# Optimization experiments

Measured on AMD Instinct MI355X. Metric: run time of the kernel, lower is better.

Reference implementation:

```python
import jax, jax.numpy as jnp
import numpy as np


def setup_inputs() -> dict:
    key = jax.random.key(0)
    ks = jax.random.split(key, 5)
    B, Lq, Lkv, HQ, H, D, S, BS = 1, 256, 4096, 32, 2, 128, 16, 64
    q = jax.random.normal(ks[0], (B, Lq, HQ, D), jnp.float32)
    k = jax.random.normal(ks[1], (B, Lkv, H, D), jnp.float32)
    v = jax.random.normal(ks[2], (B, Lkv, H, D), jnp.float32)
    w = jax.random.uniform(ks[3], (B, Lq, HQ, S), jnp.float32)
    block_indices = jax.random.randint(ks[4], (B, Lq, H, S), 0, Lkv // BS).astype(jnp.int32)
    return {"q": q, "k": k, "v": v, "w": w, "block_indices": block_indices, "block_size": BS}


def reference(q, k, v, w, block_indices, block_size):
    # q: (B, Lq, HQ, D); k,v: (B, Lkv, H, D); w: (B, Lq, HQ, num_weights);
    # block_indices: (B, Lq, H, S) int32, entries < 0 are skipped.
    B, Lq, HQ, D = q.shape
    H = k.shape[2]
    S = block_indices.shape[-1]
    G = HQ // H  # query heads per kv head
    nb = k.shape[1] // block_size
    sm_scale = 1.0 / (D ** 0.5)  # default scale in the kernel

    # Reshape KV into blocks: (B, H, nb, BS, D)
    kb = k.reshape(B, nb, block_size, H, D).transpose(0, 3, 1, 2, 4)
    vb = v.reshape(B, nb, block_size, H, D).transpose(0, 3, 1, 2, 4)

    idx = block_indices.transpose(0, 2, 1, 3)  # (B, H, Lq, S)
    valid = idx >= 0
    idx = jnp.maximum(idx, 0)

    # Gather selected blocks per (batch, kv_head): -> (B, H, Lq, S, BS, D)
    gather = jax.vmap(jax.vmap(lambda blocks, ind: blocks[ind]))
    kg = gather(kb, idx)
    vg = gather(vb, idx)

    # Group query heads by kv head: (B, H, Lq, G, D)
    qh = q.reshape(B, Lq, H, G, D).transpose(0, 2, 1, 3, 4)

    # Per-block scores and per-block softmax over the BS keys (axis u)
    scores = jnp.einsum('bhlgd,bhlsud->bhlgsu', qh, kg) * sm_scale
    p = jax.nn.softmax(scores, axis=-1)

    # Per-(head, block) learned weight; only first S weights of w are used.
    wh = w[..., :S].reshape(B, Lq, H, G, S).transpose(0, 2, 1, 3, 4)  # (B,H,Lq,G,S)
    coef = wh * valid[:, :, :, None, :].astype(p.dtype)
    p = p * coef[..., None]

    o = jnp.einsum('bhlgsu,bhlsud->bhlgd', p, vg)  # (B, H, Lq, G, D)
    return o.transpose(0, 2, 1, 3, 4).reshape(B, Lq, HQ, D)
```

## Files before the change

### kernel.cpp

```cpp
#include <hip/hip_runtime.h>
#include <hip/hip_bf16.h>


namespace {

constexpr int kLq = 256, kHQ = 32, kH = 2, kG = 16, kD = 128, kS = 16;
constexpr int kNB = 64;
constexpr float kScaleLog2e = 0.08838834764831845f * 1.4426950408889634f;

constexpr int kKPackN = kH * kNB * 16 * 64;
constexpr int kPStr   = 72;
constexpr int kSStr   = 136;

typedef short s16x8 __attribute__((ext_vector_type(8)));
typedef float f32x4 __attribute__((ext_vector_type(4)));

union U32BF2 { unsigned int u; __hip_bfloat162 h; };
union FragU  { uint4 u; s16x8 v; };

static __device__ inline unsigned int pk_bf16(float a, float b) {
    U32BF2 z; z.h = __float22bfloat162_rn(make_float2(a, b));
    return z.u;
}

__global__ __launch_bounds__(256)
void pack_kv(const float* __restrict__ k, const float* __restrict__ v,
             uint4* __restrict__ kp, uint4* __restrict__ vp)
{
    __shared__ unsigned short S_s[64 * kSStr];

    const int bid  = blockIdx.x;
    const int isV  = bid & 1;
    const int blk  = (bid >> 1) & 63;
    const int h    = bid >> 7;
    const int t    = threadIdx.x;
    const int lane = t & 63, n = lane & 15, quad = lane >> 4;
    const int wv   = t >> 6;

    {
        const float* src = (isV ? v : k) + ((size_t)blk * 64 * kH + h) * kD;
        const int r0 = t >> 5, c4 = (t & 31) << 2;
        #pragma unroll
        for (int p = 0; p < 8; ++p) {
            const int r = p * 8 + r0;
            const float4 f = *(const float4*)(src + (size_t)r * (kH * kD) + c4);
            *(unsigned int*)&S_s[r * kSStr + c4]     = pk_bf16(f.x, f.y);
            *(unsigned int*)&S_s[r * kSStr + c4 + 2] = pk_bf16(f.z, f.w);
        }
    }
    __syncthreads();

    const size_t obase = (size_t)(h * 64 + blk) * 16 * 64;
    if (!isV) {
        #pragma unroll
        for (int rep = 0; rep < 4; ++rep) {
            const int u = wv * 16 + n;
            kp[obase + (size_t)(wv * 4 + rep) * 64 + lane] =
                *(const uint4*)&S_s[u * kSStr + rep * 32 + quad * 8];
        }
    } else {
        #pragma unroll
        for (int rep = 0; rep < 4; ++rep) {
            const int c  = wv * 4 + rep;
            const int d  = (c >> 1) * 16 + n;
            const int u0 = (c & 1) * 32 + quad * 8;
            unsigned short s[8];
            #pragma unroll
            for (int j = 0; j < 8; ++j) s[j] = S_s[(u0 + j) * kSStr + d];
            uint4 val;
            val.x = s[0] | ((unsigned)s[1] << 16);
            val.y = s[2] | ((unsigned)s[3] << 16);
            val.z = s[4] | ((unsigned)s[5] << 16);
            val.w = s[6] | ((unsigned)s[7] << 16);
            vp[obase + (size_t)c * 64 + lane] = val;
        }
    }
}

__global__ __launch_bounds__(256, 2)
void hsa_main(const float* __restrict__ q, const float* __restrict__ w,
              const int* __restrict__ bidx, const uint4* __restrict__ kp,
              const uint4* __restrict__ vp, float* __restrict__ out)
{
    __shared__ __align__(16) unsigned short P_s[4 * kG * kPStr];
    __shared__ float O_red[kD * 17];

    const int bid  = blockIdx.x;
    const int l    = bid >> 1;
    const int h    = bid & 1;
    const int tid  = threadIdx.x;
    const int wave = tid >> 6;
    const int lane = tid & 63;
    const int n    = lane & 15;
    const int quad = lane >> 4;

    for (int i = tid; i < kD * 17; i += 256) O_red[i] = 0.f;

    s16x8 qf[4];
    {
        const float* qb = q + ((size_t)l * kHQ + h * kG + n) * kD + quad * 8;
        #pragma unroll
        for (int st = 0; st < 4; ++st) {
            const float4 f0 = *(const float4*)(qb + st * 32);
            const float4 f1 = *(const float4*)(qb + st * 32 + 4);
            union { s16x8 v; unsigned int u[4]; } z;
            z.u[0] = pk_bf16(f0.x, f0.y); z.u[1] = pk_bf16(f0.z, f0.w);
            z.u[2] = pk_bf16(f1.x, f1.y); z.u[3] = pk_bf16(f1.z, f1.w);
            qf[st] = z.v;
        }
    }

    const int4   bis = *(const int4*)(bidx + (size_t)(l * kH + h) * kS + wave * 4);
    const float4 wv4 = *(const float4*)(w + ((size_t)l * kHQ + h * kG + n) * kS + wave * 4);
    int   base_[4];
    float wval[4];
    {
        const int b[4] = {bis.x, bis.y, bis.z, bis.w};
        const float ww[4] = {wv4.x, wv4.y, wv4.z, wv4.w};
        #pragma unroll
        for (int j = 0; j < 4; ++j) {
            wval[j]  = (b[j] < 0) ? 0.f : ww[j];
            base_[j] = (h * kNB + max(b[j], 0)) * 16 * 64;
        }
    }

    __syncthreads();

    unsigned short* Pw = &P_s[wave * kG * kPStr];
    f32x4 oacc[8];
    #pragma unroll
    for (int dt = 0; dt < 8; ++dt) oacc[dt] = (f32x4){0.f, 0.f, 0.f, 0.f};

    FragU kreg[16];
    #pragma unroll
    for (int i = 0; i < 16; ++i) kreg[i].u = kp[base_[0] + i * 64 + lane];
    __builtin_amdgcn_sched_barrier(0);

    #pragma unroll
    for (int js = 0; js < 4; ++js) {
        FragU vreg[16];
        #pragma unroll
        for (int i = 0; i < 16; ++i) vreg[i].u = vp[base_[js] + i * 64 + lane];
        __builtin_amdgcn_sched_barrier(0);

        f32x4 sc[4];
        #pragma unroll
        for (int t = 0; t < 4; ++t) sc[t] = (f32x4){0.f, 0.f, 0.f, 0.f};
        #pragma unroll
        for (int t = 0; t < 4; ++t)
            #pragma unroll
            for (int st = 0; st < 4; ++st)
                sc[t] = __builtin_amdgcn_mfma_f32_16x16x32_bf16(
                    kreg[t * 4 + st].v, qf[st], sc[t], 0, 0, 0);

        if (js < 3) {
            #pragma unroll
            for (int i = 0; i < 16; ++i) kreg[i].u = kp[base_[js + 1] + i * 64 + lane];
        }
        __builtin_amdgcn_sched_barrier(0);

        float part = 0.f;
        #pragma unroll
        for (int t = 0; t < 4; ++t)
            #pragma unroll
            for (int r = 0; r < 4; ++r) {
                sc[t][r] = exp2f(sc[t][r] * kScaleLog2e);
                part += sc[t][r];
            }
        part += __shfl_xor(part, 16);
        part += __shfl_xor(part, 32);
        const float coef = wval[js] / part;

        #pragma unroll
        for (int t = 0; t < 4; ++t) {
            const unsigned long long pq =
                ((unsigned long long)pk_bf16(sc[t][2] * coef, sc[t][3] * coef) << 32) |
                pk_bf16(sc[t][0] * coef, sc[t][1] * coef);
            *(unsigned long long*)&Pw[n * kPStr + t * 16 + quad * 4] = pq;
        }
        const s16x8 bf0 = *(const s16x8*)&Pw[n * kPStr + quad * 8];
        const s16x8 bf1 = *(const s16x8*)&Pw[n * kPStr + 32 + quad * 8];

        #pragma unroll
        for (int dt = 0; dt < 8; ++dt) {
            oacc[dt] = __builtin_amdgcn_mfma_f32_16x16x32_bf16(
                vreg[dt * 2 + 0].v, bf0, oacc[dt], 0, 0, 0);
            oacc[dt] = __builtin_amdgcn_mfma_f32_16x16x32_bf16(
                vreg[dt * 2 + 1].v, bf1, oacc[dt], 0, 0, 0);
        }
        __builtin_amdgcn_sched_barrier(0);
    }

    #pragma unroll
    for (int dt = 0; dt < 8; ++dt)
        #pragma unroll
        for (int r = 0; r < 4; ++r)
            atomicAdd(&O_red[(dt * 16 + quad * 4 + r) * 17 + n], oacc[dt][r]);

    __syncthreads();

    {
        float* ob = out + ((size_t)l * kHQ + h * kG) * kD;
        #pragma unroll
        for (int rep = 0; rep < 2; ++rep) {
            const int idx = rep * 256 + tid;
            const int g = idx >> 5, d0 = (idx & 31) << 2;
            const float4 val = make_float4(O_red[(d0 + 0) * 17 + g],
                                           O_red[(d0 + 1) * 17 + g],
                                           O_red[(d0 + 2) * 17 + g],
                                           O_red[(d0 + 3) * 17 + g]);
            *(float4*)(ob + (size_t)g * kD + d0) = val;
        }
    }
}

}

extern "C" void kernel_launch(void* const* d_in, const int* in_sizes, int n_in,
                              void* d_out, int out_size, void* d_ws, size_t ws_size,
                              hipStream_t stream)
{
    const float* q    = (const float*)d_in[0];
    const float* k    = (const float*)d_in[1];
    const float* v    = (const float*)d_in[2];
    const float* w    = (const float*)d_in[3];
    const int*   bidx = (const int*)d_in[4];
    float* out = (float*)d_out;

    uint4* kp = (uint4*)d_ws;
    uint4* vp = (uint4*)((char*)d_ws + (size_t)kKPackN * 16);

    pack_kv<<<dim3(256), dim3(256), 0, stream>>>(k, v, kp, vp);
    hsa_main<<<dim3(kLq * kH), dim3(256), 0, stream>>>(q, w, bidx, kp, vp, out);
}
```

Before: 105.7 us.

## Double-buffer K/V blocks in LDS via async loads and split D across waves

Instead of each wave owning 4 of the 16 selected blocks and loading K/V fragments into registers, all four waves cooperatively stream each block into a double-buffered LDS staging area using global_load_lds. The next block is fetched while the current one is computed. Each wave then computes the full QK scores redundantly and owns a 32-wide slice of the output D dimension, which removes the LDS atomic cross-wave reduction and the O_red buffer. The trade-off is redundant score MFMAs and softmax in every wave, plus a block-wide barrier per selected block. The barrier between issuing the async loads and consuming the buffer relies on __syncthreads to also wait on the outstanding loads.

```diff
diff --git a/kernel.cpp b/kernel.cpp
--- a/kernel.cpp
+++ b/kernel.cpp
@@ -16,7 +16,6 @@
 typedef float f32x4 __attribute__((ext_vector_type(4)));
 
 union U32BF2 { unsigned int u; __hip_bfloat162 h; };
-union FragU  { uint4 u; s16x8 v; };
 
 static __device__ inline unsigned int pk_bf16(float a, float b) {
     U32BF2 z; z.h = __float22bfloat162_rn(make_float2(a, b));
@@ -82,8 +81,8 @@
               const int* __restrict__ bidx, const uint4* __restrict__ kp,
               const uint4* __restrict__ vp, float* __restrict__ out)
 {
+    __shared__ __align__(16) uint4 buf[2][32 * 64];
     __shared__ __align__(16) unsigned short P_s[4 * kG * kPStr];
-    __shared__ float O_red[kD * 17];
 
     const int bid  = blockIdx.x;
     const int l    = bid >> 1;
@@ -94,8 +93,6 @@
     const int n    = lane & 15;
     const int quad = lane >> 4;
 
-    for (int i = tid; i < kD * 17; i += 256) O_red[i] = 0.f;
-
     s16x8 qf[4];
     {
         const float* qb = q + ((size_t)l * kHQ + h * kG + n) * kD + quad * 8;
@@ -110,38 +107,52 @@
         }
     }
 
-    const int4   bis = *(const int4*)(bidx + (size_t)(l * kH + h) * kS + wave * 4);
-    const float4 wv4 = *(const float4*)(w + ((size_t)l * kHQ + h * kG + n) * kS + wave * 4);
-    int   base_[4];
-    float wval[4];
-    {
-        const int b[4] = {bis.x, bis.y, bis.z, bis.w};
-        const float ww[4] = {wv4.x, wv4.y, wv4.z, wv4.w};
-        #pragma unroll
-        for (int j = 0; j < 4; ++j) {
-            wval[j]  = (b[j] < 0) ? 0.f : ww[j];
-            base_[j] = (h * kNB + max(b[j], 0)) * 16 * 64;
-        }
-    }
-
+    int   base_[kS];
+    float wval[kS];
+    #pragma unroll
+    for (int i = 0; i < 4; ++i) {
+        const int4   b4 = *(const int4*)(bidx + (size_t)(l * kH + h) * kS + i * 4);
+        const float4 w4 = *(const float4*)(w + ((size_t)l * kHQ + h * kG + n) * kS + i * 4);
+        const int   bb[4] = {b4.x, b4.y, b4.z, b4.w};
+        const float ww[4] = {w4.x, w4.y, w4.z, w4.w};
+        #pragma unroll
+        for (int jj = 0; jj < 4; ++jj) {
+            wval[i * 4 + jj]  = (bb[jj] < 0) ? 0.f : ww[jj];
+            base_[i * 4 + jj] = (h * kNB + max(bb[jj], 0)) * 1024;
+        }
+    }
+
+    const int    f0    = wave * 8;
+    const uint4* gsrc  = (f0 < 16) ? kp : vp;
+    const int    fbase = (f0 < 16) ? f0 * 64 : (f0 - 16) * 64;
+
+    #define STAGE(js_, b_)                                                     \
+        {                                                                      \
+            const uint4* gp = gsrc + base_[(js_)] + fbase + lane;              \
+            auto* lp = (__attribute__((address_space(3))) uint4*)&buf[(b_)][f0 * 64]; \
+            _Pragma("unroll")                                                  \
+            for (int i_ = 0; i_ < 8; ++i_)                                     \
+                __builtin_amdgcn_global_load_lds(                              \
+                    (const __attribute__((address_space(1))) void*)(gp + i_ * 64), \
+                    (__attribute__((address_space(3))) void*)(lp + i_ * 64),   \
+                    16, 0, 0);                                                 \
+        }
+
+    STAGE(0, 0);
     __syncthreads();
 
     unsigned short* Pw = &P_s[wave * kG * kPStr];
-    f32x4 oacc[8];
+    f32x4 oacc0 = {0.f, 0.f, 0.f, 0.f};
+    f32x4 oacc1 = {0.f, 0.f, 0.f, 0.f};
+
     #pragma unroll
-    for (int dt = 0; dt < 8; ++dt) oacc[dt] = (f32x4){0.f, 0.f, 0.f, 0.f};
-
-    FragU kreg[16];
-    #pragma unroll
-    for (int i = 0; i < 16; ++i) kreg[i].u = kp[base_[0] + i * 64 + lane];
-    __builtin_amdgcn_sched_barrier(0);
-
-    #pragma unroll
-    for (int js = 0; js < 4; ++js) {
-        FragU vreg[16];
-        #pragma unroll
-        for (int i = 0; i < 16; ++i) vreg[i].u = vp[base_[js] + i * 64 + lane];
-        __builtin_amdgcn_sched_barrier(0);
+    for (int js = 0; js < kS; ++js) {
+        const int cur = js & 1;
+
+        if (js < kS - 1) {
+            STAGE(js + 1, cur ^ 1);
+            __builtin_amdgcn_sched_barrier(0);
+        }
 
         f32x4 sc[4];
         #pragma unroll
@@ -149,15 +160,10 @@
         #pragma unroll
         for (int t = 0; t < 4; ++t)
             #pragma unroll
-            for (int st = 0; st < 4; ++st)
-                sc[t] = __builtin_amdgcn_mfma_f32_16x16x32_bf16(
-                    kreg[t * 4 + st].v, qf[st], sc[t], 0, 0, 0);
-
-        if (js < 3) {
-            #pragma unroll
-            for (int i = 0; i < 16; ++i) kreg[i].u = kp[base_[js + 1] + i * 64 + lane];
-        }
-        __builtin_amdgcn_sched_barrier(0);
+            for (int st = 0; st < 4; ++st) {
+                const s16x8 af = *(const s16x8*)&buf[cur][(t * 4 + st) * 64 + lane];
+                sc[t] = __builtin_amdgcn_mfma_f32_16x16x32_bf16(af, qf[st], sc[t], 0, 0, 0);
+            }
 
         float part = 0.f;
         #pragma unroll
@@ -181,36 +187,27 @@
         const s16x8 bf0 = *(const s16x8*)&Pw[n * kPStr + quad * 8];
         const s16x8 bf1 = *(const s16x8*)&Pw[n * kPStr + 32 + quad * 8];
 
-        #pragma unroll
-        for (int dt = 0; dt < 8; ++dt) {
-            oacc[dt] = __builtin_amdgcn_mfma_f32_16x16x32_bf16(
-                vreg[dt * 2 + 0].v, bf0, oacc[dt], 0, 0, 0);
-            oacc[dt] = __builtin_amdgcn_mfma_f32_16x16x32_bf16(
-                vreg[dt * 2 + 1].v, bf1, oacc[dt], 0, 0, 0);
-        }
-        __builtin_amdgcn_sched_barrier(0);
-    }
-
-    #pragma unroll
-    for (int dt = 0; dt < 8; ++dt)
-        #pragma unroll
-        for (int r = 0; r < 4; ++r)
-            atomicAdd(&O_red[(dt * 16 + quad * 4 + r) * 17 + n], oacc[dt][r]);
-
-    __syncthreads();
+        {
+            const int dt0 = wave * 2;
+            const s16x8 a00 = *(const s16x8*)&buf[cur][(16 + dt0 * 2 + 0) * 64 + lane];
+            const s16x8 a01 = *(const s16x8*)&buf[cur][(16 + dt0 * 2 + 1) * 64 + lane];
+            oacc0 = __builtin_amdgcn_mfma_f32_16x16x32_bf16(a00, bf0, oacc0, 0, 0, 0);
+            oacc0 = __builtin_amdgcn_mfma_f32_16x16x32_bf16(a01, bf1, oacc0, 0, 0, 0);
+            const s16x8 a10 = *(const s16x8*)&buf[cur][(16 + dt0 * 2 + 2) * 64 + lane];
+            const s16x8 a11 = *(const s16x8*)&buf[cur][(16 + dt0 * 2 + 3) * 64 + lane];
+            oacc1 = __builtin_amdgcn_mfma_f32_16x16x32_bf16(a10, bf0, oacc1, 0, 0, 0);
+            oacc1 = __builtin_amdgcn_mfma_f32_16x16x32_bf16(a11, bf1, oacc1, 0, 0, 0);
+        }
+
+        __syncthreads();
+    }
+    #undef STAGE
 
     {
-        float* ob = out + ((size_t)l * kHQ + h * kG) * kD;
-        #pragma unroll
-        for (int rep = 0; rep < 2; ++rep) {
-            const int idx = rep * 256 + tid;
-            const int g = idx >> 5, d0 = (idx & 31) << 2;
-            const float4 val = make_float4(O_red[(d0 + 0) * 17 + g],
-                                           O_red[(d0 + 1) * 17 + g],
-                                           O_red[(d0 + 2) * 17 + g],
-                                           O_red[(d0 + 3) * 17 + g]);
-            *(float4*)(ob + (size_t)g * kD + d0) = val;
-        }
+        float* ob = out + ((size_t)l * kHQ + h * kG + n) * kD;
+        const int d0 = wave * 32 + quad * 4;
+        *(float4*)(ob + d0)      = make_float4(oacc0[0], oacc0[1], oacc0[2], oacc0[3]);
+        *(float4*)(ob + d0 + 16) = make_float4(oacc1[0], oacc1[1], oacc1[2], oacc1[3]);
     }
 }
 
```

Result: faster. 102.1 us (-3.5%).
